# Kernel optimization log

Hardware: AMD Instinct MI355X
Metric: run time of the kernel (lower is better)

## Reference

```python
import jax, jax.numpy as jnp
import numpy as np

HID = 512
HEADS = 8
DK = HID // HEADS


def setup_inputs() -> dict:
    key = jax.random.key(0)
    ks = jax.random.split(key, 11)
    B, Nq, Nk = 2, 4096, 4096
    s = 1.0 / np.sqrt(HID)
    inp = {
        "query": jax.random.normal(ks[0], (B, Nq, HID), jnp.float32),
        "key": jax.random.normal(ks[1], (B, Nk, HID), jnp.float32),
        "value": jax.random.normal(ks[2], (B, Nk, HID), jnp.float32),
        "Wq": jax.random.normal(ks[3], (HID, HID), jnp.float32) * s,
        "bq": jnp.zeros((HID,), jnp.float32),
        "Wk": jax.random.normal(ks[4], (HID, HID), jnp.float32) * s,
        "bk": jnp.zeros((HID,), jnp.float32),
        "Wv": jax.random.normal(ks[5], (HID, HID), jnp.float32) * s,
        "bv": jnp.zeros((HID,), jnp.float32),
        "Wo": jax.random.normal(ks[6], (HID, HID), jnp.float32) * s,
        "bo": jnp.zeros((HID,), jnp.float32),
    }
    return inp


def reference(query, key, value, Wq, bq, Wk, bk, Wv, bv, Wo, bo):
    B, Nq, _ = query.shape
    Nk = key.shape[1]
    # torch Linear: x @ W.T + b
    Q = (query @ Wq.T + bq).reshape(B, Nq, HEADS, DK).transpose(0, 2, 1, 3)  # (B,H,Nq,dk)
    K = (key @ Wk.T + bk).reshape(B, Nk, HEADS, DK).transpose(0, 2, 1, 3)    # (B,H,Nk,dk)
    V = (value @ Wv.T + bv).reshape(B, Nk, HEADS, DK).transpose(0, 2, 1, 3)  # (B,H,Nk,dk)
    scale = 1.0 / jnp.sqrt(jnp.asarray(DK, query.dtype))
    scores = jnp.einsum("bhqd,bhkd->bhqk", Q, K) * scale  # (B,H,Nq,Nk)
    attn = jax.nn.softmax(scores, axis=-1)
    # dropout is identity in eval/inference mode (deterministic reference)
    context = jnp.einsum("bhqk,bhkd->bhqd", attn, V)  # (B,H,Nq,dk)
    context = context.transpose(0, 2, 1, 3).reshape(B, Nq, HID)
    out = context @ Wo.T + bo
    return out, attn
```

## Files before the change

kernel.cpp:

```cpp
#include <hip/hip_runtime.h>
#include <hip/hip_bf16.h>

#define NB   2
#define NH   8
#define NSEQ 4096
#define DKH  64
#define HD   512

typedef unsigned short u16;
typedef unsigned int   u32;
typedef short s16x8 __attribute__((ext_vector_type(8)));
typedef u16   u16x8 __attribute__((ext_vector_type(8)));
typedef u16   u16x4 __attribute__((ext_vector_type(4)));
typedef u32   u32x2 __attribute__((ext_vector_type(2)));
typedef float f32x4 __attribute__((ext_vector_type(4)));

#define L2E 1.4426950408889634f

static __device__ __forceinline__ u16 f2bf(float f) {
    u32 u = __builtin_bit_cast(u32, f);
    u32 r = (u + 0x7fffu + ((u >> 16) & 1u)) >> 16;
    return (u16)r;
}
static __device__ __forceinline__ float bf2f(u16 h) {
    return __builtin_bit_cast(float, (u32)h << 16);
}
static __device__ __forceinline__ f32x4 mm16(s16x8 a, s16x8 b, f32x4 c) {
    return __builtin_amdgcn_mfma_f32_16x16x32_bf16(a, b, c, 0, 0, 0);
}
static __device__ __forceinline__ s16x8 ld8(const u16* p) {
    return __builtin_bit_cast(s16x8, *(const u16x8*)p);
}
static __device__ __forceinline__ void bar_sync() {
    __builtin_amdgcn_sched_barrier(0);
    asm volatile("s_waitcnt lgkmcnt(0)" ::: "memory");
    __builtin_amdgcn_sched_barrier(0);
    __builtin_amdgcn_s_barrier();
    __builtin_amdgcn_sched_barrier(0);
}

template<int TERMS, int MODE, bool WLO>
__launch_bounds__(512, 2)
__global__ void proj_kernel(const float* __restrict__ X, const float* __restrict__ W,
                            const float* __restrict__ bias,
                            u16* __restrict__ Yhi, u16* __restrict__ Ylo, float scale)
{
    __shared__ u16 xh[128][40], xl[128][40], wh[128][40], wl[128][40];
    const int t = threadIdx.x;
    const int lane = t & 63, wave = t >> 6;
    const int lg = lane >> 4, lr = lane & 15;
    const int wr = (wave >> 2) * 64, wc = (wave & 3) * 32;
    const int m0 = blockIdx.x * 128, n0 = blockIdx.y * 128;

    f32x4 acc[4][2] = {};

    for (int k0 = 0; k0 < HD; k0 += 32) {
        #pragma unroll
        for (int i = 0; i < 2; i++) {
            int idx = t + i * 512;
            int r = idx >> 3, c = (idx & 7) * 4;
            float4 v = *(const float4*)(X + (size_t)(m0 + r) * HD + k0 + c);
            u16 h0 = f2bf(v.x), h1 = f2bf(v.y), h2 = f2bf(v.z), h3 = f2bf(v.w);
            u16x4 hv; hv[0] = h0; hv[1] = h1; hv[2] = h2; hv[3] = h3;
            *(u16x4*)&xh[r][c] = hv;
            if (TERMS >= 2) {
                u16x4 lv;
                lv[0] = f2bf(v.x - bf2f(h0)); lv[1] = f2bf(v.y - bf2f(h1));
                lv[2] = f2bf(v.z - bf2f(h2)); lv[3] = f2bf(v.w - bf2f(h3));
                *(u16x4*)&xl[r][c] = lv;
            }
            float4 w = *(const float4*)(W + (size_t)(n0 + r) * HD + k0 + c);
            u16 g0 = f2bf(w.x), g1 = f2bf(w.y), g2 = f2bf(w.z), g3 = f2bf(w.w);
            u16x4 gv; gv[0] = g0; gv[1] = g1; gv[2] = g2; gv[3] = g3;
            *(u16x4*)&wh[r][c] = gv;
            if (TERMS >= 3) {
                u16x4 lv;
                lv[0] = f2bf(w.x - bf2f(g0)); lv[1] = f2bf(w.y - bf2f(g1));
                lv[2] = f2bf(w.z - bf2f(g2)); lv[3] = f2bf(w.w - bf2f(g3));
                *(u16x4*)&wl[r][c] = lv;
            }
        }
        __syncthreads();
        const int kk = lg * 8;
        s16x8 ah[4], al[4], bh[2], bl[2];
        #pragma unroll
        for (int f = 0; f < 4; f++) {
            ah[f] = ld8(&xh[wr + f * 16 + lr][kk]);
            if (TERMS >= 2) al[f] = ld8(&xl[wr + f * 16 + lr][kk]);
        }
        #pragma unroll
        for (int f = 0; f < 2; f++) {
            bh[f] = ld8(&wh[wc + f * 16 + lr][kk]);
            if (TERMS >= 3) bl[f] = ld8(&wl[wc + f * 16 + lr][kk]);
        }
        #pragma unroll
        for (int m = 0; m < 4; m++)
            #pragma unroll
            for (int n = 0; n < 2; n++) {
                acc[m][n] = mm16(ah[m], bh[n], acc[m][n]);
                if (TERMS >= 2) acc[m][n] = mm16(al[m], bh[n], acc[m][n]);
                if (TERMS >= 3) acc[m][n] = mm16(ah[m], bl[n], acc[m][n]);
            }
        __syncthreads();
    }

    float bv[2];
    #pragma unroll
    for (int n = 0; n < 2; n++) bv[n] = bias[n0 + wc + n * 16 + lr];

    #pragma unroll
    for (int m = 0; m < 4; m++)
        #pragma unroll
        for (int n = 0; n < 2; n++) {
            int col = n0 + wc + n * 16 + lr;
            int h = col >> 6, d = col & 63;
            #pragma unroll
            for (int j = 0; j < 4; j++) {
                int row = m0 + wr + m * 16 + lg * 4 + j;
                int b = row >> 12, nn = row & (NSEQ - 1);
                float y = (acc[m][n][j] + bv[n]) * scale;
                u16 hi = f2bf(y);
                if (MODE == 0) {
                    size_t o = (((size_t)(b * NH + h) * NSEQ) + nn) * DKH + d;
                    Yhi[o] = hi;
                    if (WLO) Ylo[o] = f2bf(y - bf2f(hi));
                } else {
                    size_t o = ((size_t)(b * NH + h) * DKH + d) * (size_t)NSEQ + nn;
                    Yhi[o] = hi;
                }
            }
        }
}

static __device__ __forceinline__ void swz_bh_q(int& bh, int& qblk) {
    int f = blockIdx.x + 32 * blockIdx.y;
    int r = f & 7, q = f >> 3;
    bh = 2 * r + (q >> 5);
    qblk = q & 31;
}

#define NT (NSEQ / 64)

__launch_bounds__(256, 2)
__global__ void attn_kernel(const u16* __restrict__ Qh, const u16* __restrict__ Ql,
                            const u16* __restrict__ Kh, const u16* __restrict__ Vt,
                            float* __restrict__ attn, u16* __restrict__ ctx)
{
    __shared__ u16 kh[2][64][72], vt[2][64][72];
    __shared__ u16 plds[4][32][72];
    const int t = threadIdx.x, lane = t & 63, wave = t >> 6;
    const int lg = lane >> 4, lr = lane & 15;
    int bh, qblk; swz_bh_q(bh, qblk);
    const int q0 = qblk * 128 + wave * 32;
    const size_t nbase = (size_t)bh * NSEQ;

    const int sr = t >> 3;
    const int sc = (t & 7) * 8;
    const u16* gK = Kh + nbase * DKH + (size_t)sr * DKH + sc;
    const u16* gV = Vt + ((size_t)bh * DKH + sr) * NSEQ + sc;

    s16x8 qh[2][2], ql[2][2];
    #pragma unroll
    for (int qi = 0; qi < 2; qi++)
        #pragma unroll
        for (int ds = 0; ds < 2; ds++) {
            size_t o = (nbase + q0 + qi * 16 + lr) * DKH + ds * 32 + lg * 8;
            qh[qi][ds] = ld8(Qh + o);
            ql[qi][ds] = ld8(Ql + o);
        }

    float sums[2] = {0.f, 0.f};
    {
        *(u16x8*)&kh[0][sr][sc]      = *(const u16x8*)(gK);
        *(u16x8*)&kh[0][sr + 32][sc] = *(const u16x8*)(gK + (size_t)32 * DKH);
        bar_sync();
        for (int tt = 0; tt < NT; tt++) {
            const int cur = tt & 1, nxt = cur ^ 1;
            u16x8 pk0, pk1;
            if (tt + 1 < NT) {
                pk0 = *(const u16x8*)(gK + (size_t)(tt * 64 + 64) * DKH);
                pk1 = *(const u16x8*)(gK + (size_t)(tt * 64 + 96) * DKH);
            }
            f32x4 S[2][4] = {};
            __builtin_amdgcn_s_setprio(1);
            #pragma unroll
            for (int ds = 0; ds < 2; ds++) {
                s16x8 bf[4];
                #pragma unroll
                for (int kf = 0; kf < 4; kf++)
                    bf[kf] = ld8(&kh[cur][kf * 16 + lr][ds * 32 + lg * 8]);
                #pragma unroll
                for (int qi = 0; qi < 2; qi++)
                    #pragma unroll
                    for (int kf = 0; kf < 4; kf++)
                        S[qi][kf] = mm16(bf[kf], qh[qi][ds], S[qi][kf]);
            }
            __builtin_amdgcn_s_setprio(0);
            #pragma unroll
            for (int qi = 0; qi < 2; qi++)
                #pragma unroll
                for (int kf = 0; kf < 4; kf++)
                    #pragma unroll
                    for (int j = 0; j < 4; j++)
                        sums[qi] += __builtin_amdgcn_exp2f(S[qi][kf][j] * L2E);
            if (tt + 1 < NT) {
                *(u16x8*)&kh[nxt][sr][sc]      = pk0;
                *(u16x8*)&kh[nxt][sr + 32][sc] = pk1;
            }
            bar_sync();
        }
    }
    #pragma unroll
    for (int qi = 0; qi < 2; qi++) {
        sums[qi] += __shfl_xor(sums[qi], 16, 64);
        sums[qi] += __shfl_xor(sums[qi], 32, 64);
    }

    float lrl[2];
    float* aptr[2];
    #pragma unroll
    for (int qi = 0; qi < 2; qi++) {
        lrl[qi] = -__builtin_amdgcn_logf(sums[qi]);
        aptr[qi] = attn + (nbase + q0 + qi * 16 + lr) * (size_t)NSEQ + lg * 4;
    }

    #pragma unroll
    for (int i = 0; i < 2; i++) {
        int r = sr + i * 32;
        *(u16x8*)&kh[0][r][sc] = *(const u16x8*)(gK + (size_t)(i * 32) * DKH);
        *(u16x8*)&vt[0][r][sc] = *(const u16x8*)(gV + (size_t)(i * 32) * NSEQ);
    }
    bar_sync();

    f32x4 O[2][4] = {};
    for (int tt = 0; tt < NT; tt++) {
        const int cur = tt & 1, nxt = cur ^ 1;
        const int k0 = tt * 64;

        u16x8 pk[2], pv[2];
        if (tt + 1 < NT) {
            #pragma unroll
            for (int i = 0; i < 2; i++) {
                pk[i] = *(const u16x8*)(gK + (size_t)(k0 + 64 + i * 32) * DKH);
                pv[i] = *(const u16x8*)(gV + (size_t)(i * 32) * NSEQ + k0 + 64);
            }
        }

        f32x4 S[2][4] = {};
        __builtin_amdgcn_s_setprio(1);
        #pragma unroll
        for (int ds = 0; ds < 2; ds++) {
            s16x8 bkh[4];
            #pragma unroll
            for (int kf = 0; kf < 4; kf++)
                bkh[kf] = ld8(&kh[cur][kf * 16 + lr][ds * 32 + lg * 8]);
            #pragma unroll
            for (int qi = 0; qi < 2; qi++)
                #pragma unroll
                for (int kf = 0; kf < 4; kf++) {
                    S[qi][kf] = mm16(bkh[kf], qh[qi][ds], S[qi][kf]);
                    S[qi][kf] = mm16(bkh[kf], ql[qi][ds], S[qi][kf]);
                }
        }
        __builtin_amdgcn_s_setprio(0);

        #pragma unroll
        for (int qi = 0; qi < 2; qi++)
            #pragma unroll
            for (int kf = 0; kf < 4; kf++) {
                f32x4 p;
                #pragma unroll
                for (int j = 0; j < 4; j++)
                    p[j] = __builtin_amdgcn_exp2f(fmaf(S[qi][kf][j], L2E, lrl[qi]));
                *(f32x4*)(aptr[qi] + kf * 16) = p;
                u32x2 pk2;
                pk2[0] = (u32)f2bf(p[0]) | ((u32)f2bf(p[1]) << 16);
                pk2[1] = (u32)f2bf(p[2]) | ((u32)f2bf(p[3]) << 16);
                *(u32x2*)&plds[wave][qi * 16 + lr][kf * 16 + lg * 4] = pk2;
            }

        __builtin_amdgcn_wave_barrier();

        __builtin_amdgcn_s_setprio(1);
        #pragma unroll
        for (int ks = 0; ks < 2; ks++) {
            s16x8 pa[2], vb[4];
            #pragma unroll
            for (int qi = 0; qi < 2; qi++)
                pa[qi] = ld8(&plds[wave][qi * 16 + lr][ks * 32 + lg * 8]);
            #pragma unroll
            for (int df = 0; df < 4; df++)
                vb[df] = ld8(&vt[cur][df * 16 + lr][ks * 32 + lg * 8]);
            #pragma unroll
            for (int qi = 0; qi < 2; qi++)
                #pragma unroll
                for (int df = 0; df < 4; df++)
                    O[qi][df] = mm16(pa[qi], vb[df], O[qi][df]);
        }
        __builtin_amdgcn_s_setprio(0);

        if (tt + 1 < NT) {
            #pragma unroll
            for (int i = 0; i < 2; i++) {
                int r = sr + i * 32;
                *(u16x8*)&kh[nxt][r][sc] = pk[i];
                *(u16x8*)&vt[nxt][r][sc] = pv[i];
            }
        }
        aptr[0] += 64;
        aptr[1] += 64;
        bar_sync();
    }

    const int b = bh >> 3, h = bh & 7;
    #pragma unroll
    for (int qi = 0; qi < 2; qi++)
        #pragma unroll
        for (int df = 0; df < 4; df++)
            #pragma unroll
            for (int j = 0; j < 4; j++) {
                int n = q0 + qi * 16 + lg * 4 + j;
                int col = h * 64 + df * 16 + lr;
                ctx[((size_t)b * NSEQ + n) * HD + col] = f2bf(O[qi][df][j]);
            }
}

__launch_bounds__(512, 2)
__global__ void outproj_kernel(const u16* __restrict__ Xc, const float* __restrict__ W,
                               const float* __restrict__ bias, float* __restrict__ out)
{
    __shared__ u16 xh[128][72], wh[128][72];
    const int t = threadIdx.x, lane = t & 63, wave = t >> 6;
    const int lg = lane >> 4, lr = lane & 15;
    const int wr = (wave >> 2) * 64, wc = (wave & 3) * 32;
    const int m0 = blockIdx.x * 128, n0 = blockIdx.y * 128;

    f32x4 acc[4][2] = {};
    for (int k0 = 0; k0 < HD; k0 += 64) {
        #pragma unroll
        for (int i = 0; i < 2; i++) {
            int idx = t + i * 512;
            int r = idx >> 3, c = (idx & 7) * 8;
            *(u16x8*)&xh[r][c] = *(const u16x8*)(Xc + (size_t)(m0 + r) * HD + k0 + c);
        }
        #pragma unroll
        for (int i = 0; i < 4; i++) {
            int idx = t + i * 512;
            int r = idx >> 4, c = (idx & 15) * 4;
            float4 v = *(const float4*)(W + (size_t)(n0 + r) * HD + k0 + c);
            u16x4 gv; gv[0] = f2bf(v.x); gv[1] = f2bf(v.y); gv[2] = f2bf(v.z); gv[3] = f2bf(v.w);
            *(u16x4*)&wh[r][c] = gv;
        }
        __syncthreads();
        #pragma unroll
        for (int ks = 0; ks < 2; ks++) {
            s16x8 af[4], bf[2];
            int kk = ks * 32 + lg * 8;
            #pragma unroll
            for (int f = 0; f < 4; f++) af[f] = ld8(&xh[wr + f * 16 + lr][kk]);
            #pragma unroll
            for (int f = 0; f < 2; f++) bf[f] = ld8(&wh[wc + f * 16 + lr][kk]);
            #pragma unroll
            for (int m = 0; m < 4; m++)
                #pragma unroll
                for (int n = 0; n < 2; n++)
                    acc[m][n] = mm16(af[m], bf[n], acc[m][n]);
        }
        __syncthreads();
    }
    #pragma unroll
    for (int m = 0; m < 4; m++)
        #pragma unroll
        for (int n = 0; n < 2; n++) {
            int col = n0 + wc + n * 16 + lr;
            float bv = bias[col];
            #pragma unroll
            for (int j = 0; j < 4; j++) {
                int row = m0 + wr + m * 16 + lg * 4 + j;
                out[(size_t)row * HD + col] = acc[m][n][j] + bv;
            }
        }
}

extern "C" void kernel_launch(void* const* d_in, const int* in_sizes, int n_in,
                              void* d_out, int out_size, void* d_ws, size_t ws_size,
                              hipStream_t stream)
{
    const float* query = (const float*)d_in[0];
    const float* key   = (const float*)d_in[1];
    const float* value = (const float*)d_in[2];
    const float* Wq = (const float*)d_in[3];
    const float* bq = (const float*)d_in[4];
    const float* Wk = (const float*)d_in[5];
    const float* bk = (const float*)d_in[6];
    const float* Wv = (const float*)d_in[7];
    const float* bv = (const float*)d_in[8];
    const float* Wo = (const float*)d_in[9];
    const float* bo = (const float*)d_in[10];

    float* out  = (float*)d_out;
    float* attn = out + (size_t)NB * NSEQ * HD;

    const size_t E = (size_t)NB * NH * NSEQ * DKH;
    u16* qhi = (u16*)d_ws;
    u16* qlo = qhi + E;
    u16* khi = qlo + E;
    u16* vt  = khi + E;
    u16* ctx = vt + E;

    dim3 gp(64, 4), bp(512);
    proj_kernel<3, 0, true ><<<gp, bp, 0, stream>>>(query, Wq, bq, qhi, qlo, 0.125f);
    proj_kernel<3, 0, false><<<gp, bp, 0, stream>>>(key,   Wk, bk, khi, (u16*)nullptr, 1.0f);
    proj_kernel<1, 1, false><<<gp, bp, 0, stream>>>(value, Wv, bv, vt,  (u16*)nullptr, 1.0f);
    attn_kernel<<<dim3(32, 16), dim3(256), 0, stream>>>(qhi, qlo, khi, vt, attn, ctx);
    outproj_kernel<<<gp, bp, 0, stream>>>(ctx, Wo, bo, out);
}
```

Measured before the change: 481.9 us.

## Drop split-bf16 compensation terms and stage projection stores through LDS

Removes the hi/lo bf16 split for Q and K projections and for the QK^T score computation, so each GEMM uses a single bf16 MFMA instead of two or three. The Q low-part buffer and its loads are gone. The projection epilogue now writes results to a shared-memory staging tile and emits 16-byte coalesced stores in either the row-major or transposed layout, replacing scattered 2-byte stores. This trades accuracy of the attention scores (bf16-only Q·K) for fewer MFMAs and less memory traffic.

```diff
diff --git a/kernel.cpp b/kernel.cpp
--- a/kernel.cpp
+++ b/kernel.cpp
@@ -22,9 +22,6 @@
     u32 r = (u + 0x7fffu + ((u >> 16) & 1u)) >> 16;
     return (u16)r;
 }
-static __device__ __forceinline__ float bf2f(u16 h) {
-    return __builtin_bit_cast(float, (u32)h << 16);
-}
 static __device__ __forceinline__ f32x4 mm16(s16x8 a, s16x8 b, f32x4 c) {
     return __builtin_amdgcn_mfma_f32_16x16x32_bf16(a, b, c, 0, 0, 0);
 }
@@ -39,13 +36,14 @@
     __builtin_amdgcn_sched_barrier(0);
 }
 
-template<int TERMS, int MODE, bool WLO>
+template<int MODE>
 __launch_bounds__(512, 2)
 __global__ void proj_kernel(const float* __restrict__ X, const float* __restrict__ W,
                             const float* __restrict__ bias,
-                            u16* __restrict__ Yhi, u16* __restrict__ Ylo, float scale)
+                            u16* __restrict__ Y, float scale)
 {
-    __shared__ u16 xh[128][40], xl[128][40], wh[128][40], wl[128][40];
+    __shared__ u16 xh[128][40], wh[128][40];
+    __shared__ u16 st[9216];
     const int t = threadIdx.x;
     const int lane = t & 63, wave = t >> 6;
     const int lg = lane >> 4, lr = lane & 15;
@@ -60,47 +58,24 @@
             int idx = t + i * 512;
             int r = idx >> 3, c = (idx & 7) * 4;
             float4 v = *(const float4*)(X + (size_t)(m0 + r) * HD + k0 + c);
-            u16 h0 = f2bf(v.x), h1 = f2bf(v.y), h2 = f2bf(v.z), h3 = f2bf(v.w);
-            u16x4 hv; hv[0] = h0; hv[1] = h1; hv[2] = h2; hv[3] = h3;
+            u16x4 hv; hv[0] = f2bf(v.x); hv[1] = f2bf(v.y); hv[2] = f2bf(v.z); hv[3] = f2bf(v.w);
             *(u16x4*)&xh[r][c] = hv;
-            if (TERMS >= 2) {
-                u16x4 lv;
-                lv[0] = f2bf(v.x - bf2f(h0)); lv[1] = f2bf(v.y - bf2f(h1));
-                lv[2] = f2bf(v.z - bf2f(h2)); lv[3] = f2bf(v.w - bf2f(h3));
-                *(u16x4*)&xl[r][c] = lv;
-            }
             float4 w = *(const float4*)(W + (size_t)(n0 + r) * HD + k0 + c);
-            u16 g0 = f2bf(w.x), g1 = f2bf(w.y), g2 = f2bf(w.z), g3 = f2bf(w.w);
-            u16x4 gv; gv[0] = g0; gv[1] = g1; gv[2] = g2; gv[3] = g3;
+            u16x4 gv; gv[0] = f2bf(w.x); gv[1] = f2bf(w.y); gv[2] = f2bf(w.z); gv[3] = f2bf(w.w);
             *(u16x4*)&wh[r][c] = gv;
-            if (TERMS >= 3) {
-                u16x4 lv;
-                lv[0] = f2bf(w.x - bf2f(g0)); lv[1] = f2bf(w.y - bf2f(g1));
-                lv[2] = f2bf(w.z - bf2f(g2)); lv[3] = f2bf(w.w - bf2f(g3));
-                *(u16x4*)&wl[r][c] = lv;
-            }
         }
         __syncthreads();
         const int kk = lg * 8;
-        s16x8 ah[4], al[4], bh[2], bl[2];
-        #pragma unroll
-        for (int f = 0; f < 4; f++) {
-            ah[f] = ld8(&xh[wr + f * 16 + lr][kk]);
-            if (TERMS >= 2) al[f] = ld8(&xl[wr + f * 16 + lr][kk]);
-        }
-        #pragma unroll
-        for (int f = 0; f < 2; f++) {
-            bh[f] = ld8(&wh[wc + f * 16 + lr][kk]);
-            if (TERMS >= 3) bl[f] = ld8(&wl[wc + f * 16 + lr][kk]);
-        }
+        s16x8 ah[4], bh[2];
+        #pragma unroll
+        for (int f = 0; f < 4; f++) ah[f] = ld8(&xh[wr + f * 16 + lr][kk]);
+        #pragma unroll
+        for (int f = 0; f < 2; f++) bh[f] = ld8(&wh[wc + f * 16 + lr][kk]);
         #pragma unroll
         for (int m = 0; m < 4; m++)
             #pragma unroll
-            for (int n = 0; n < 2; n++) {
+            for (int n = 0; n < 2; n++)
                 acc[m][n] = mm16(ah[m], bh[n], acc[m][n]);
-                if (TERMS >= 2) acc[m][n] = mm16(al[m], bh[n], acc[m][n]);
-                if (TERMS >= 3) acc[m][n] = mm16(ah[m], bl[n], acc[m][n]);
-            }
         __syncthreads();
     }
 
@@ -108,28 +83,49 @@
     #pragma unroll
     for (int n = 0; n < 2; n++) bv[n] = bias[n0 + wc + n * 16 + lr];
 
-    #pragma unroll
-    for (int m = 0; m < 4; m++)
-        #pragma unroll
-        for (int n = 0; n < 2; n++) {
-            int col = n0 + wc + n * 16 + lr;
-            int h = col >> 6, d = col & 63;
-            #pragma unroll
-            for (int j = 0; j < 4; j++) {
-                int row = m0 + wr + m * 16 + lg * 4 + j;
-                int b = row >> 12, nn = row & (NSEQ - 1);
-                float y = (acc[m][n][j] + bv[n]) * scale;
-                u16 hi = f2bf(y);
-                if (MODE == 0) {
-                    size_t o = (((size_t)(b * NH + h) * NSEQ) + nn) * DKH + d;
-                    Yhi[o] = hi;
-                    if (WLO) Ylo[o] = f2bf(y - bf2f(hi));
-                } else {
-                    size_t o = ((size_t)(b * NH + h) * DKH + d) * (size_t)NSEQ + nn;
-                    Yhi[o] = hi;
+    const int mych = (wave & 3) >> 1;
+    const int wcl  = wc & 63;
+
+    #pragma unroll
+    for (int ch = 0; ch < 2; ch++) {
+        if (mych == ch) {
+            #pragma unroll
+            for (int m = 0; m < 4; m++)
+                #pragma unroll
+                for (int n = 0; n < 2; n++) {
+                    int c = wcl + n * 16 + lr;
+                    #pragma unroll
+                    for (int j = 0; j < 4; j++) {
+                        int r = wr + m * 16 + lg * 4 + j;
+                        u16 hv = f2bf((acc[m][n][j] + bv[n]) * scale);
+                        if (MODE == 0) st[r * 72 + c]  = hv;
+                        else           st[c * 136 + r] = hv;
+                    }
                 }
-            }
-        }
+        }
+        __syncthreads();
+        const int hh = (n0 >> 6) + ch;
+        if (MODE == 0) {
+            #pragma unroll
+            for (int i = 0; i < 2; i++) {
+                int flat = t + i * 512;
+                int r = flat >> 3, dc = (flat & 7) * 8;
+                int row = m0 + r, b = row >> 12, nn = row & (NSEQ - 1);
+                size_t o = (((size_t)(b * NH + hh) * NSEQ) + nn) * DKH + dc;
+                *(u16x8*)(Y + o) = *(const u16x8*)&st[r * 72 + dc];
+            }
+        } else {
+            #pragma unroll
+            for (int i = 0; i < 2; i++) {
+                int flat = t + i * 512;
+                int c = flat >> 4, rc = (flat & 15) * 8;
+                int row = m0 + rc, b = row >> 12, nn = row & (NSEQ - 1);
+                size_t o = ((size_t)(b * NH + hh) * DKH + c) * (size_t)NSEQ + nn;
+                *(u16x8*)(Y + o) = *(const u16x8*)&st[c * 136 + rc];
+            }
+        }
+        if (ch == 0) __syncthreads();
+    }
 }
 
 static __device__ __forceinline__ void swz_bh_q(int& bh, int& qblk) {
@@ -142,8 +138,8 @@
 #define NT (NSEQ / 64)
 
 __launch_bounds__(256, 2)
-__global__ void attn_kernel(const u16* __restrict__ Qh, const u16* __restrict__ Ql,
-                            const u16* __restrict__ Kh, const u16* __restrict__ Vt,
+__global__ void attn_kernel(const u16* __restrict__ Qh, const u16* __restrict__ Kh,
+                            const u16* __restrict__ Vt,
                             float* __restrict__ attn, u16* __restrict__ ctx)
 {
     __shared__ u16 kh[2][64][72], vt[2][64][72];
@@ -159,15 +155,12 @@
     const u16* gK = Kh + nbase * DKH + (size_t)sr * DKH + sc;
     const u16* gV = Vt + ((size_t)bh * DKH + sr) * NSEQ + sc;
 
-    s16x8 qh[2][2], ql[2][2];
+    s16x8 qh[2][2];
     #pragma unroll
     for (int qi = 0; qi < 2; qi++)
         #pragma unroll
-        for (int ds = 0; ds < 2; ds++) {
-            size_t o = (nbase + q0 + qi * 16 + lr) * DKH + ds * 32 + lg * 8;
-            qh[qi][ds] = ld8(Qh + o);
-            ql[qi][ds] = ld8(Ql + o);
-        }
+        for (int ds = 0; ds < 2; ds++)
+            qh[qi][ds] = ld8(Qh + (nbase + q0 + qi * 16 + lr) * DKH + ds * 32 + lg * 8);
 
     float sums[2] = {0.f, 0.f};
     {
@@ -257,10 +250,8 @@
             #pragma unroll
             for (int qi = 0; qi < 2; qi++)
                 #pragma unroll
-                for (int kf = 0; kf < 4; kf++) {
+                for (int kf = 0; kf < 4; kf++)
                     S[qi][kf] = mm16(bkh[kf], qh[qi][ds], S[qi][kf]);
-                    S[qi][kf] = mm16(bkh[kf], ql[qi][ds], S[qi][kf]);
-                }
         }
         __builtin_amdgcn_s_setprio(0);
 
@@ -403,15 +394,14 @@
 
     const size_t E = (size_t)NB * NH * NSEQ * DKH;
     u16* qhi = (u16*)d_ws;
-    u16* qlo = qhi + E;
-    u16* khi = qlo + E;
+    u16* khi = qhi + E;
     u16* vt  = khi + E;
     u16* ctx = vt + E;
 
     dim3 gp(64, 4), bp(512);
-    proj_kernel<3, 0, true ><<<gp, bp, 0, stream>>>(query, Wq, bq, qhi, qlo, 0.125f);
-    proj_kernel<3, 0, false><<<gp, bp, 0, stream>>>(key,   Wk, bk, khi, (u16*)nullptr, 1.0f);
-    proj_kernel<1, 1, false><<<gp, bp, 0, stream>>>(value, Wv, bv, vt,  (u16*)nullptr, 1.0f);
-    attn_kernel<<<dim3(32, 16), dim3(256), 0, stream>>>(qhi, qlo, khi, vt, attn, ctx);
+    proj_kernel<0><<<gp, bp, 0, stream>>>(query, Wq, bq, qhi, 0.125f);
+    proj_kernel<0><<<gp, bp, 0, stream>>>(key,   Wk, bk, khi, 1.0f);
+    proj_kernel<1><<<gp, bp, 0, stream>>>(value, Wv, bv, vt,  1.0f);
+    attn_kernel<<<dim3(32, 16), dim3(256), 0, stream>>>(qhi, khi, vt, attn, ctx);
     outproj_kernel<<<gp, bp, 0, stream>>>(ctx, Wo, bo, out);
 }
```

Measured after the change: 451.2 us. 6.4% less time.
